# Performance work log

Measured on AMD Instinct MI355X. Metric: run time of the kernel, lower is better.

## Reference

```python
import jax, jax.numpy as jnp
import numpy as np

D_K = 32
N_HEADS = 16


def setup_inputs() -> dict:
    key = jax.random.key(0)
    ks = jax.random.split(key, 11)
    B, S, F = 32, 2048, 128
    d_k, d_v, filt = 32, 32, 3
    return {
        "q_in": jax.random.normal(ks[0], (B, S, F), jnp.float32),
        "k_in": jax.random.normal(ks[1], (B, S, F), jnp.float32),
        "v_in": jax.random.normal(ks[2], (B, S, F), jnp.float32),
        "Wq": jax.random.normal(ks[3], (F, d_k), jnp.float32) * 0.05,
        "bq": jax.random.normal(ks[4], (d_k,), jnp.float32) * 0.05,
        "Wk": jax.random.normal(ks[5], (F, d_k), jnp.float32) * 0.05,
        "bk": jax.random.normal(ks[6], (d_k,), jnp.float32) * 0.05,
        "Wv": jax.random.normal(ks[7], (F, d_v), jnp.float32) * 0.05,
        "bv": jax.random.normal(ks[8], (d_v,), jnp.float32) * 0.05,
        "Wo": jax.random.normal(ks[9], (N_HEADS * d_v, filt), jnp.float32) * 0.05,
        "bo": jax.random.normal(ks[10], (filt,), jnp.float32) * 0.05,
    }


def reference(q_in, k_in, v_in, Wq, bq, Wk, bk, Wv, bv, Wo, bo):
    # SingleAttention: Dense projections then scaled dot-product attention.
    q = q_in @ Wq + bq            # [B,S,d_k]
    k = k_in @ Wk + bk            # [B,S,d_k]
    v = v_in @ Wv + bv            # [B,S,d_v]
    scores = jnp.einsum('bqd,bkd->bqk', q, k) / jnp.sqrt(jnp.float32(D_K))
    attn = jax.nn.softmax(scores, axis=-1)
    head = jnp.einsum('bqk,bkd->bqd', attn, v)  # [B,S,d_v]
    # Original uses [SingleAttention()]*n_heads -> all heads are the SAME layer,
    # so the concat is n_heads identical copies of one head output.
    combined = jnp.tile(head, (1, 1, N_HEADS))   # [B,S,n_heads*d_v]
    return combined @ Wo + bo                    # [B,S,filter_size]
```

## Files before the change

kernel.cpp:

```cpp
#include <hip/hip_runtime.h>
#include <stdint.h>

using f16 = _Float16;
typedef _Float16 f16x8 __attribute__((ext_vector_type(8)));
typedef _Float16 f16x4 __attribute__((ext_vector_type(4)));
typedef float f32x4 __attribute__((ext_vector_type(4)));

constexpr int Bn    = 32;
constexpr int Sn    = 2048;
constexpr int Fn    = 128;
constexpr int DKn   = 32;
constexpr int NHn   = 16;
constexpr int FILTn = 3;
constexpr int Mn    = Bn * Sn;

constexpr float QSCALE = 0.1767766952966369f * 1.4426950408889634f;

constexpr int MISC_WOEFF = 0;
constexpr int MISC_BO    = 96;
constexpr int MISC_BQ    = 99;
constexpr int MISC_BK    = 131;
constexpr int MISC_BV    = 163;

#define ASYNC_COPY16(gp, lp)                                                   \
    __builtin_amdgcn_global_load_lds(                                          \
        (const __attribute__((address_space(1))) uint32_t*)(const void*)(gp),  \
        (__attribute__((address_space(3))) uint32_t*)(lp), 16, 0, 0)

#define WAIT_VM2 __builtin_amdgcn_s_waitcnt(0xF72)
#define WAIT_VM0 __builtin_amdgcn_s_waitcnt(0xF70)

__global__ __launch_bounds__(256) void prep_kernel(
    const float* __restrict__ Wq, const float* __restrict__ bq,
    const float* __restrict__ Wk, const float* __restrict__ bk,
    const float* __restrict__ Wv, const float* __restrict__ bv,
    const float* __restrict__ Wo, const float* __restrict__ bo,
    f16* __restrict__ wtg, float* __restrict__ misc)
{
    for (int idx = blockIdx.x * 256 + threadIdx.x; idx < 3 * 4096;
         idx += gridDim.x * 256) {
        const int T    = idx >> 12;
        const int r    = idx & 4095;
        const int nt   = r >> 11;
        const int ks   = (r >> 9) & 3;
        const int lane = (r >> 3) & 63;
        const int j    = r & 7;
        const int k    = ks * 32 + (lane >> 4) * 8 + j;
        const int c    = nt * 16 + (lane & 15);
        const float* W = (T == 0) ? Wq : ((T == 1) ? Wk : Wv);
        const float sc = (T == 0) ? QSCALE : 1.0f;
        wtg[idx] = (f16)(W[k * DKn + c] * sc);
    }
    if (blockIdx.x == 0) {
        const int t = threadIdx.x;
        if (t < 96) {
            const int d = t / 3, f = t - 3 * d;
            float s = 0.f;
#pragma unroll
            for (int h = 0; h < NHn; ++h) s += Wo[(h * DKn + d) * FILTn + f];
            misc[MISC_WOEFF + t] = s;
        } else if (t < 99) {
            misc[MISC_BO + (t - 96)] = bo[t - 96];
        } else if (t < 131) {
            misc[MISC_BQ + (t - 99)] = bq[t - 99] * QSCALE;
        } else if (t < 163) {
            misc[MISC_BK + (t - 131)] = bk[t - 131];
        } else if (t < 195) {
            misc[MISC_BV + (t - 163)] = bv[t - 163];
        }
    }
}

__global__ __launch_bounds__(256) void qkv_proj(
    const float* __restrict__ q_in, const float* __restrict__ k_in,
    const float* __restrict__ v_in,
    const f16* __restrict__ wtg, const float* __restrict__ misc,
    f16* __restrict__ q_ws, f16* __restrict__ k_ws, f16* __restrict__ v_ws)
{
    const int t    = threadIdx.x;
    const int w    = t >> 6;
    const int lane = t & 63;
    const int n    = lane & 15;
    const int quad = lane >> 4;
    const int T    = blockIdx.x / 512;
    const int rowA = (((blockIdx.x - T * 512) * 4 + w)) * 32;
    const int rowB = rowA + 16;
    const float* in = (T == 0) ? q_in : ((T == 1) ? k_in : v_in);

    f16x8 wf[2][4];
#pragma unroll
    for (int nt = 0; nt < 2; ++nt)
#pragma unroll
        for (int ks = 0; ks < 4; ++ks)
            wf[nt][ks] =
                *(const f16x8*)(wtg + T * 4096 + (nt * 4 + ks) * 512 + lane * 8);

    f16x8 afA[4], afB[4];
#pragma unroll
    for (int ks = 0; ks < 4; ++ks) {
        const float* pA = in + (size_t)(rowA + n) * Fn + ks * 32 + quad * 8;
        const float* pB = in + (size_t)(rowB + n) * Fn + ks * 32 + quad * 8;
        const float4 a0 = *(const float4*)pA;
        const float4 a1 = *(const float4*)(pA + 4);
        const float4 b0 = *(const float4*)pB;
        const float4 b1 = *(const float4*)(pB + 4);
        f16x8 a, b;
        a[0]=(f16)a0.x; a[1]=(f16)a0.y; a[2]=(f16)a0.z; a[3]=(f16)a0.w;
        a[4]=(f16)a1.x; a[5]=(f16)a1.y; a[6]=(f16)a1.z; a[7]=(f16)a1.w;
        b[0]=(f16)b0.x; b[1]=(f16)b0.y; b[2]=(f16)b0.z; b[3]=(f16)b0.w;
        b[4]=(f16)b1.x; b[5]=(f16)b1.y; b[6]=(f16)b1.z; b[7]=(f16)b1.w;
        afA[ks] = a;
        afB[ks] = b;
    }

    if (T < 2) {
        const float* bb = misc + (T == 0 ? MISC_BQ : MISC_BK);
        const float b0 = bb[n], b1 = bb[16 + n];
        f32x4 accA0 = {b0, b0, b0, b0}, accA1 = {b1, b1, b1, b1};
        f32x4 accB0 = {b0, b0, b0, b0}, accB1 = {b1, b1, b1, b1};
#pragma unroll
        for (int ks = 0; ks < 4; ++ks) {
            accA0 = __builtin_amdgcn_mfma_f32_16x16x32_f16(afA[ks], wf[0][ks], accA0, 0, 0, 0);
            accA1 = __builtin_amdgcn_mfma_f32_16x16x32_f16(afA[ks], wf[1][ks], accA1, 0, 0, 0);
            accB0 = __builtin_amdgcn_mfma_f32_16x16x32_f16(afB[ks], wf[0][ks], accB0, 0, 0, 0);
            accB1 = __builtin_amdgcn_mfma_f32_16x16x32_f16(afB[ks], wf[1][ks], accB1, 0, 0, 0);
        }
        f16* ows = (T == 0) ? q_ws : k_ws;
#pragma unroll
        for (int r = 0; r < 4; ++r) {
            const int ra = rowA + quad * 4 + r;
            const int rb = rowB + quad * 4 + r;
            ows[(size_t)ra * DKn + n]      = (f16)accA0[r];
            ows[(size_t)ra * DKn + 16 + n] = (f16)accA1[r];
            ows[(size_t)rb * DKn + n]      = (f16)accB0[r];
            ows[(size_t)rb * DKn + 16 + n] = (f16)accB1[r];
        }
    } else {
        f32x4 accA0 = {0.f,0.f,0.f,0.f}, accA1 = {0.f,0.f,0.f,0.f};
        f32x4 accB0 = {0.f,0.f,0.f,0.f}, accB1 = {0.f,0.f,0.f,0.f};
#pragma unroll
        for (int ks = 0; ks < 4; ++ks) {
            accA0 = __builtin_amdgcn_mfma_f32_16x16x32_f16(wf[0][ks], afA[ks], accA0, 0, 0, 0);
            accA1 = __builtin_amdgcn_mfma_f32_16x16x32_f16(wf[1][ks], afA[ks], accA1, 0, 0, 0);
            accB0 = __builtin_amdgcn_mfma_f32_16x16x32_f16(wf[0][ks], afB[ks], accB0, 0, 0, 0);
            accB1 = __builtin_amdgcn_mfma_f32_16x16x32_f16(wf[1][ks], afB[ks], accB1, 0, 0, 0);
        }
        const int b  = rowA >> 11;
        const int sA = (rowA & (Sn - 1)) + n;
        const int sB = sA + 16;
#pragma unroll
        for (int r = 0; r < 4; ++r) {
            const int d0 = quad * 4 + r;
            v_ws[((size_t)(b * DKn + d0)) * Sn + sA] =
                (f16)(accA0[r] + misc[MISC_BV + d0]);
            v_ws[((size_t)(b * DKn + 16 + d0)) * Sn + sA] =
                (f16)(accA1[r] + misc[MISC_BV + 16 + d0]);
            v_ws[((size_t)(b * DKn + d0)) * Sn + sB] =
                (f16)(accB0[r] + misc[MISC_BV + d0]);
            v_ws[((size_t)(b * DKn + 16 + d0)) * Sn + sB] =
                (f16)(accB1[r] + misc[MISC_BV + 16 + d0]);
        }
    }
}

__global__ __launch_bounds__(256, 4) void flash_mfma(
    const f16* __restrict__ q_ws, const f16* __restrict__ k_ws,
    const f16* __restrict__ v_ws,
    const float* __restrict__ misc, float* __restrict__ out)
{
    __shared__ f16 kv[3][2][2048];

    const int t    = threadIdx.x;
    const int w    = t >> 6;
    const int lane = t & 63;
    const int n    = lane & 15;
    const int quad = lane >> 4;
    const int b    = (blockIdx.x & 7) * 4 + (blockIdx.x >> 8);
    const int qt   = (blockIdx.x >> 3) & 31;

    const f16* Ksrc = k_ws + (size_t)b * Sn * DKn
                    + (size_t)(t >> 2) * DKn + (((t & 3) ^ ((t >> 3) & 3)) * 8);
    const f16* Vsrc = v_ws + (size_t)b * DKn * Sn
                    + (size_t)(t >> 3) * Sn + (((t & 7) ^ ((t >> 3) & 7)) * 8);

#define STAGE(KT, BUF)                                              \
    {                                                               \
        ASYNC_COPY16(Ksrc + (size_t)(KT) * 2048, &kv[BUF][0][w * 512]); \
        ASYNC_COPY16(Vsrc + (size_t)(KT) * 64,   &kv[BUF][1][w * 512]); \
    }

    const int qrow0 = b * Sn + qt * 64 + w * 16;
    const f16x8 qa = *(const f16x8*)(q_ws + (size_t)(qrow0 + n) * DKn + quad * 8);

    int koff[4];
#pragma unroll
    for (int g = 0; g < 4; ++g)
        koff[g] = (g * 64 + n * 4 + (quad ^ ((n >> 1) & 3))) * 8;

    int voff2[2][4];
#pragma unroll
    for (int h = 0; h < 2; ++h)
#pragma unroll
        for (int s = 0; s < 4; ++s) {
            const int d  = h * 16 + n;
            const int jc = s * 2 + (quad >> 1);
            voff2[h][s] = (d * 8 + (jc ^ (d & 7))) * 8 + (quad & 1) * 4;
        }

    f32x4 o0 = {0.f, 0.f, 0.f, 0.f};
    f32x4 o1 = {0.f, 0.f, 0.f, 0.f};
    float lsum = 0.f;
    const f32x4 zero = {0.f, 0.f, 0.f, 0.f};

    STAGE(0, 0)
    STAGE(1, 1)

#pragma unroll 1
    for (int kt = 0; kt < Sn / 64; ++kt) {
        const int cur = kt % 3;
        WAIT_VM2;
        __builtin_amdgcn_s_barrier();
        STAGE((kt + 2) & 31, (kt + 2) % 3)

        const f16* Kt = &kv[cur][0][0];
        const f16* Vt = &kv[cur][1][0];

        const f16x8 kb0 = *(const f16x8*)(Kt + koff[0]);
        const f16x8 kb1 = *(const f16x8*)(Kt + koff[1]);
        const f16x8 kb2 = *(const f16x8*)(Kt + koff[2]);
        const f16x8 kb3 = *(const f16x8*)(Kt + koff[3]);
        f16x4 vb[2][4];
#pragma unroll
        for (int h = 0; h < 2; ++h)
#pragma unroll
            for (int s = 0; s < 4; ++s)
                vb[h][s] = *(const f16x4*)(Vt + voff2[h][s]);

        const f32x4 s0 = __builtin_amdgcn_mfma_f32_16x16x32_f16(kb0, qa, zero, 0, 0, 0);
        const f32x4 s1 = __builtin_amdgcn_mfma_f32_16x16x32_f16(kb1, qa, zero, 0, 0, 0);
        const f32x4 s2 = __builtin_amdgcn_mfma_f32_16x16x32_f16(kb2, qa, zero, 0, 0, 0);
        const f32x4 s3 = __builtin_amdgcn_mfma_f32_16x16x32_f16(kb3, qa, zero, 0, 0, 0);

        f16x4 pa[4];
#pragma unroll
        for (int g = 0; g < 4; ++g) {
            const f32x4 sg = (g == 0) ? s0 : ((g == 1) ? s1 : ((g == 2) ? s2 : s3));
            const float p0 = __builtin_amdgcn_exp2f(sg[0]);
            const float p1 = __builtin_amdgcn_exp2f(sg[1]);
            const float p2 = __builtin_amdgcn_exp2f(sg[2]);
            const float p3 = __builtin_amdgcn_exp2f(sg[3]);
            lsum += (p0 + p1) + (p2 + p3);
            f16x4 pp;
            pp[0] = (f16)p0; pp[1] = (f16)p1; pp[2] = (f16)p2; pp[3] = (f16)p3;
            pa[g] = pp;
        }

#pragma unroll
        for (int s = 0; s < 4; ++s) {
            o0 = __builtin_amdgcn_mfma_f32_16x16x16f16(pa[s], vb[0][s], o0, 0, 0, 0);
            o1 = __builtin_amdgcn_mfma_f32_16x16x16f16(pa[s], vb[1][s], o1, 0, 0, 0);
        }
    }
#undef STAGE
    WAIT_VM0;

    float lf = lsum;
    lf += __shfl_xor(lf, 16);
    lf += __shfl_xor(lf, 32);

    float w0f[FILTn], w1f[FILTn];
#pragma unroll
    for (int f = 0; f < FILTn; ++f) {
        w0f[f] = misc[MISC_WOEFF + n * FILTn + f];
        w1f[f] = misc[MISC_WOEFF + (16 + n) * FILTn + f];
    }
#pragma unroll
    for (int r = 0; r < 4; ++r) {
        const float inv = 1.f / __shfl(lf, quad * 4 + r);
        const float a0 = o0[r] * inv;
        const float a1 = o1[r] * inv;
#pragma unroll
        for (int f = 0; f < FILTn; ++f) {
            float v = a0 * w0f[f] + a1 * w1f[f];
            v += __shfl_xor(v, 1, 16);
            v += __shfl_xor(v, 2, 16);
            v += __shfl_xor(v, 4, 16);
            v += __shfl_xor(v, 8, 16);
            if (n == f) {
                const int row = qrow0 + quad * 4 + r;
                out[(size_t)row * FILTn + f] = v + misc[MISC_BO + f];
            }
        }
    }
}

extern "C" void kernel_launch(void* const* d_in, const int* in_sizes, int n_in,
                              void* d_out, int out_size, void* d_ws,
                              size_t ws_size, hipStream_t stream)
{
    const float* q_in = (const float*)d_in[0];
    const float* k_in = (const float*)d_in[1];
    const float* v_in = (const float*)d_in[2];
    const float* Wq   = (const float*)d_in[3];
    const float* bq   = (const float*)d_in[4];
    const float* Wk   = (const float*)d_in[5];
    const float* bk   = (const float*)d_in[6];
    const float* Wv   = (const float*)d_in[7];
    const float* bv   = (const float*)d_in[8];
    const float* Wo   = (const float*)d_in[9];
    const float* bo   = (const float*)d_in[10];
    float* out = (float*)d_out;

    f16*   ws   = (f16*)d_ws;
    f16*   q_ws = ws;
    f16*   k_ws = ws + (size_t)Mn * DKn;
    f16*   v_ws = ws + 2 * (size_t)Mn * DKn;
    f16*   wtg  = ws + 3 * (size_t)Mn * DKn;
    float* misc = (float*)(wtg + 3 * 4096);

    prep_kernel<<<16, 256, 0, stream>>>(Wq, bq, Wk, bk, Wv, bv, Wo, bo, wtg, misc);

    qkv_proj<<<3 * 512, 256, 0, stream>>>(
        q_in, k_in, v_in, wtg, misc, q_ws, k_ws, v_ws);

    flash_mfma<<<Bn * (Sn / 64), 256, 0, stream>>>(
        q_ws, k_ws, v_ws, misc, out);
}
```

Baseline: 177.3 us.

## Process two 16-row query groups per wave to reuse K/V tiles

Each wave now handles 32 query rows instead of 16, so a block covers 128 queries and the grid is halved. Every K/V tile staged in LDS and every K/V fragment read from LDS now feeds twice the MFMA and exp work. This cuts global and LDS traffic per unit of compute. In exchange it doubles the accumulator and probability registers and relaxes launch bounds to 2 blocks per CU, which lowers occupancy and leaves fewer blocks to fill the GPU.

```diff
diff --git a/kernel.cpp b/kernel.cpp
--- a/kernel.cpp
+++ b/kernel.cpp
@@ -163,7 +163,7 @@
     }
 }
 
-__global__ __launch_bounds__(256, 4) void flash_mfma(
+__global__ __launch_bounds__(256, 2) void flash_mfma(
     const f16* __restrict__ q_ws, const f16* __restrict__ k_ws,
     const f16* __restrict__ v_ws,
     const float* __restrict__ misc, float* __restrict__ out)
@@ -175,8 +175,8 @@
     const int lane = t & 63;
     const int n    = lane & 15;
     const int quad = lane >> 4;
-    const int b    = (blockIdx.x & 7) * 4 + (blockIdx.x >> 8);
-    const int qt   = (blockIdx.x >> 3) & 31;
+    const int b    = (blockIdx.x & 7) * 4 + (blockIdx.x >> 7);
+    const int qt   = (blockIdx.x >> 3) & 15;
 
     const f16* Ksrc = k_ws + (size_t)b * Sn * DKn
                     + (size_t)(t >> 2) * DKn + (((t & 3) ^ ((t >> 3) & 3)) * 8);
@@ -189,8 +189,9 @@
         ASYNC_COPY16(Vsrc + (size_t)(KT) * 64,   &kv[BUF][1][w * 512]); \
     }
 
-    const int qrow0 = b * Sn + qt * 64 + w * 16;
-    const f16x8 qa = *(const f16x8*)(q_ws + (size_t)(qrow0 + n) * DKn + quad * 8);
+    const int qrow0 = b * Sn + qt * 128 + w * 32;
+    const f16x8 qa0 = *(const f16x8*)(q_ws + (size_t)(qrow0 + n) * DKn + quad * 8);
+    const f16x8 qa1 = *(const f16x8*)(q_ws + (size_t)(qrow0 + 16 + n) * DKn + quad * 8);
 
     int koff[4];
 #pragma unroll
@@ -207,9 +208,11 @@
             voff2[h][s] = (d * 8 + (jc ^ (d & 7))) * 8 + (quad & 1) * 4;
         }
 
-    f32x4 o0 = {0.f, 0.f, 0.f, 0.f};
-    f32x4 o1 = {0.f, 0.f, 0.f, 0.f};
-    float lsum = 0.f;
+    f32x4 o00 = {0.f, 0.f, 0.f, 0.f};
+    f32x4 o01 = {0.f, 0.f, 0.f, 0.f};
+    f32x4 o10 = {0.f, 0.f, 0.f, 0.f};
+    f32x4 o11 = {0.f, 0.f, 0.f, 0.f};
+    float l0 = 0.f, l1 = 0.f;
     const f32x4 zero = {0.f, 0.f, 0.f, 0.f};
 
     STAGE(0, 0)
@@ -236,37 +239,53 @@
             for (int s = 0; s < 4; ++s)
                 vb[h][s] = *(const f16x4*)(Vt + voff2[h][s]);
 
-        const f32x4 s0 = __builtin_amdgcn_mfma_f32_16x16x32_f16(kb0, qa, zero, 0, 0, 0);
-        const f32x4 s1 = __builtin_amdgcn_mfma_f32_16x16x32_f16(kb1, qa, zero, 0, 0, 0);
-        const f32x4 s2 = __builtin_amdgcn_mfma_f32_16x16x32_f16(kb2, qa, zero, 0, 0, 0);
-        const f32x4 s3 = __builtin_amdgcn_mfma_f32_16x16x32_f16(kb3, qa, zero, 0, 0, 0);
-
-        f16x4 pa[4];
-#pragma unroll
-        for (int g = 0; g < 4; ++g) {
-            const f32x4 sg = (g == 0) ? s0 : ((g == 1) ? s1 : ((g == 2) ? s2 : s3));
-            const float p0 = __builtin_amdgcn_exp2f(sg[0]);
-            const float p1 = __builtin_amdgcn_exp2f(sg[1]);
-            const float p2 = __builtin_amdgcn_exp2f(sg[2]);
-            const float p3 = __builtin_amdgcn_exp2f(sg[3]);
-            lsum += (p0 + p1) + (p2 + p3);
-            f16x4 pp;
-            pp[0] = (f16)p0; pp[1] = (f16)p1; pp[2] = (f16)p2; pp[3] = (f16)p3;
-            pa[g] = pp;
-        }
+        f16x4 pa0[4], pa1[4];
+#define QK_GROUP(g, kbg)                                                       \
+        {                                                                      \
+            const f32x4 sa =                                                   \
+                __builtin_amdgcn_mfma_f32_16x16x32_f16(kbg, qa0, zero, 0, 0, 0);\
+            const f32x4 sb =                                                   \
+                __builtin_amdgcn_mfma_f32_16x16x32_f16(kbg, qa1, zero, 0, 0, 0);\
+            const float a0 = __builtin_amdgcn_exp2f(sa[0]);                    \
+            const float a1 = __builtin_amdgcn_exp2f(sa[1]);                    \
+            const float a2 = __builtin_amdgcn_exp2f(sa[2]);                    \
+            const float a3 = __builtin_amdgcn_exp2f(sa[3]);                    \
+            l0 += (a0 + a1) + (a2 + a3);                                       \
+            f16x4 ppa;                                                         \
+            ppa[0] = (f16)a0; ppa[1] = (f16)a1;                                \
+            ppa[2] = (f16)a2; ppa[3] = (f16)a3;                                \
+            pa0[g] = ppa;                                                      \
+            const float b0 = __builtin_amdgcn_exp2f(sb[0]);                    \
+            const float b1 = __builtin_amdgcn_exp2f(sb[1]);                    \
+            const float b2 = __builtin_amdgcn_exp2f(sb[2]);                    \
+            const float b3 = __builtin_amdgcn_exp2f(sb[3]);                    \
+            l1 += (b0 + b1) + (b2 + b3);                                       \
+            f16x4 ppb;                                                         \
+            ppb[0] = (f16)b0; ppb[1] = (f16)b1;                                \
+            ppb[2] = (f16)b2; ppb[3] = (f16)b3;                                \
+            pa1[g] = ppb;                                                      \
+        }
+        QK_GROUP(0, kb0)
+        QK_GROUP(1, kb1)
+        QK_GROUP(2, kb2)
+        QK_GROUP(3, kb3)
+#undef QK_GROUP
 
 #pragma unroll
         for (int s = 0; s < 4; ++s) {
-            o0 = __builtin_amdgcn_mfma_f32_16x16x16f16(pa[s], vb[0][s], o0, 0, 0, 0);
-            o1 = __builtin_amdgcn_mfma_f32_16x16x16f16(pa[s], vb[1][s], o1, 0, 0, 0);
+            o00 = __builtin_amdgcn_mfma_f32_16x16x16f16(pa0[s], vb[0][s], o00, 0, 0, 0);
+            o01 = __builtin_amdgcn_mfma_f32_16x16x16f16(pa0[s], vb[1][s], o01, 0, 0, 0);
+            o10 = __builtin_amdgcn_mfma_f32_16x16x16f16(pa1[s], vb[0][s], o10, 0, 0, 0);
+            o11 = __builtin_amdgcn_mfma_f32_16x16x16f16(pa1[s], vb[1][s], o11, 0, 0, 0);
         }
     }
 #undef STAGE
     WAIT_VM0;
 
-    float lf = lsum;
-    lf += __shfl_xor(lf, 16);
-    lf += __shfl_xor(lf, 32);
+    l0 += __shfl_xor(l0, 16);
+    l0 += __shfl_xor(l0, 32);
+    l1 += __shfl_xor(l1, 16);
+    l1 += __shfl_xor(l1, 32);
 
     float w0f[FILTn], w1f[FILTn];
 #pragma unroll
@@ -275,20 +294,26 @@
         w1f[f] = misc[MISC_WOEFF + (16 + n) * FILTn + f];
     }
 #pragma unroll
-    for (int r = 0; r < 4; ++r) {
-        const float inv = 1.f / __shfl(lf, quad * 4 + r);
-        const float a0 = o0[r] * inv;
-        const float a1 = o1[r] * inv;
-#pragma unroll
-        for (int f = 0; f < FILTn; ++f) {
-            float v = a0 * w0f[f] + a1 * w1f[f];
-            v += __shfl_xor(v, 1, 16);
-            v += __shfl_xor(v, 2, 16);
-            v += __shfl_xor(v, 4, 16);
-            v += __shfl_xor(v, 8, 16);
-            if (n == f) {
-                const int row = qrow0 + quad * 4 + r;
-                out[(size_t)row * FILTn + f] = v + misc[MISC_BO + f];
+    for (int qg = 0; qg < 2; ++qg) {
+        const float lf = (qg == 0) ? l0 : l1;
+        const f32x4 oA = (qg == 0) ? o00 : o10;
+        const f32x4 oB = (qg == 0) ? o01 : o11;
+#pragma unroll
+        for (int r = 0; r < 4; ++r) {
+            const float inv = 1.f / __shfl(lf, quad * 4 + r);
+            const float a0 = oA[r] * inv;
+            const float a1 = oB[r] * inv;
+#pragma unroll
+            for (int f = 0; f < FILTn; ++f) {
+                float v = a0 * w0f[f] + a1 * w1f[f];
+                v += __shfl_xor(v, 1, 16);
+                v += __shfl_xor(v, 2, 16);
+                v += __shfl_xor(v, 4, 16);
+                v += __shfl_xor(v, 8, 16);
+                if (n == f) {
+                    const int row = qrow0 + qg * 16 + quad * 4 + r;
+                    out[(size_t)row * FILTn + f] = v + misc[MISC_BO + f];
+                }
             }
         }
     }
@@ -323,6 +348,6 @@
     qkv_proj<<<3 * 512, 256, 0, stream>>>(
         q_in, k_in, v_in, wtg, misc, q_ws, k_ws, v_ws);
 
-    flash_mfma<<<Bn * (Sn / 64), 256, 0, stream>>>(
+    flash_mfma<<<Bn * (Sn / 128), 256, 0, stream>>>(
         q_ws, k_ws, v_ws, misc, out);
 }
```

Result: no change. 175.5 us (-1.0%).
